# Kernel tuning notes

Measured on AMD Instinct MI355X. Metric: run time of the kernel, lower is better.

The kernel has to match this reference:

```python
import jax, jax.numpy as jnp
import numpy as np

NEG_SLOPE = 0.2  # PyG GATConv default leaky_relu slope


def _gat_conv(x, src, dst, W, a_src, a_dst, b, num_nodes):
    # Linear transform: [N, F_out]
    h = x @ W
    # Per-node attention halves (heads=1): [N]
    alpha_s = h @ a_src
    alpha_d = h @ a_dst
    # Per-edge raw score for edge j->i: a_src.h_j + a_dst.h_i
    e = jax.nn.leaky_relu(alpha_s[src] + alpha_d[dst], NEG_SLOPE)
    # Softmax over edges grouped by destination node (numerically stable)
    m = jax.ops.segment_max(e, dst, num_segments=num_nodes)
    ex = jnp.exp(e - m[dst])
    denom = jax.ops.segment_sum(ex, dst, num_segments=num_nodes)
    coef = ex / denom[dst]
    # Attention-weighted aggregation of source features into destinations
    out = jax.ops.segment_sum(h[src] * coef[:, None], dst, num_segments=num_nodes)
    return out + b


def setup_inputs() -> dict:
    key = jax.random.key(0)
    ks = jax.random.split(key, 12)
    N, F_in, F_hid, F_out, E = 100000, 128, 64, 40, 1600000
    x = jax.random.normal(ks[0], (N, F_in), dtype=jnp.float32)
    edge_index = jax.random.randint(ks[1], (2, E), 0, N, dtype=jnp.int64)
    g = lambda k, shape, fan: jax.random.normal(k, shape, dtype=jnp.float32) * (1.0 / np.sqrt(fan))
    return {
        "x": x,
        "edge_index": edge_index,
        "W1": g(ks[2], (F_in, F_hid), F_in),
        "a_src1": g(ks[3], (F_hid,), F_hid),
        "a_dst1": g(ks[4], (F_hid,), F_hid),
        "b1": jnp.zeros((F_hid,), dtype=jnp.float32),
        "W2": g(ks[5], (F_hid, F_out), F_hid),
        "a_src2": g(ks[6], (F_out,), F_out),
        "a_dst2": g(ks[7], (F_out,), F_out),
        "b2": jnp.zeros((F_out,), dtype=jnp.float32),
    }


def reference(x, edge_index, W1, a_src1, a_dst1, b1, W2, a_src2, a_dst2, b2):
    N = x.shape[0]
    # PyG GATConv adds self loops by default
    loops = jnp.arange(N, dtype=edge_index.dtype)
    src = jnp.concatenate([edge_index[0], loops])
    dst = jnp.concatenate([edge_index[1], loops])
    h = _gat_conv(x, src, dst, W1, a_src1, a_dst1, b1, N)
    h = jax.nn.relu(h)
    # dropout p=0.5 is inactive in eval mode
    h = _gat_conv(h, src, dst, W2, a_src2, a_dst2, b2, N)
    return jax.nn.log_softmax(h, axis=-1)
```

## Files before the change

### kernel.cpp

```cpp
#include <hip/hip_runtime.h>
#include <math.h>


constexpr int F_IN = 128;
constexpr int F_H  = 64;
constexpr int F_O  = 40;
constexpr int NBMAX = 512;
constexpr int CHUNK = 8192;
constexpr int NKEY  = 2048;

using h2 = decltype(__builtin_amdgcn_cvt_pkrtz(0.f, 0.f));
typedef __attribute__((ext_vector_type(4))) float f32x4;
typedef __attribute__((ext_vector_type(8))) short s16x8;

__device__ __forceinline__ h2 u2h(unsigned u) { return __builtin_bit_cast(h2, u); }

__device__ __forceinline__ float fdot2f(h2 a, h2 b, float c) {
#if __has_builtin(__builtin_amdgcn_fdot2)
    return __builtin_amdgcn_fdot2(a, b, c, false);
#else
    return c + (float)a.x * (float)b.x + (float)a.y * (float)b.y;
#endif
}
__device__ __forceinline__ h2 pklo(unsigned a, unsigned b) {
    return u2h(__builtin_amdgcn_perm(a, b, 0x05040100u));
}
__device__ __forceinline__ h2 pkhi(unsigned a, unsigned b) {
    return u2h(__builtin_amdgcn_perm(a, b, 0x07060302u));
}
__device__ __forceinline__ unsigned short f2h(float f) {
    _Float16 x = (_Float16)f;
    return __builtin_bit_cast(unsigned short, x);
}


__global__ __launch_bounds__(256) void k_binA(const int* __restrict__ dsts,
                                              int* __restrict__ bcnt,
                                              int E, int Et, int NB) {
    __shared__ int hist[NBMAX];
    for (int i = threadIdx.x; i < NB; i += 256) hist[i] = 0;
    __syncthreads();
    int e0 = blockIdx.x * 2048;
#pragma unroll
    for (int it = 0; it < 8; ++it) {
        int e = e0 + it * 256 + threadIdx.x;
        if (e < Et) {
            int d = (e < E) ? dsts[e] : (e - E);
            atomicAdd(&hist[d >> 8], 1);
        }
    }
    __syncthreads();
    for (int i = threadIdx.x; i < NB; i += 256) {
        int c = hist[i];
        if (c) atomicAdd(&bcnt[i], c);
    }
}

__global__ __launch_bounds__(NBMAX) void k_binB(const int* __restrict__ bcnt,
                                                int* __restrict__ bbase,
                                                int* __restrict__ bcur,
                                                int* __restrict__ rp,
                                                int NB, int N, int Et) {
    __shared__ int sc[NBMAX];
    int t = threadIdx.x;
    int v = (t < NB) ? bcnt[t] : 0;
    sc[t] = v; __syncthreads();
    int x = v;
    for (int o = 1; o < NBMAX; o <<= 1) {
        int y = (t >= o) ? sc[t - o] : 0;
        __syncthreads();
        x += y;
        sc[t] = x;
        __syncthreads();
    }
    if (t < NB) { int b = x - v; bbase[t] = b; bcur[t] = b; }
    if (t == 0) rp[N] = Et;
}

__global__ __launch_bounds__(256) void k_binC(const int* __restrict__ srcs,
                                              const int* __restrict__ dsts,
                                              int* __restrict__ bcur,
                                              unsigned* __restrict__ binned,
                                              int E, int Et, int NB) {
    __shared__ int hist[NBMAX];
    __shared__ int gbase[NBMAX];
    __shared__ int lcnt[NBMAX];
    int t = threadIdx.x;
    for (int i = t; i < NB; i += 256) hist[i] = 0;
    __syncthreads();
    int e0 = blockIdx.x * CHUNK;
#pragma unroll 4
    for (int it = 0; it < CHUNK / 256; ++it) {
        int e = e0 + it * 256 + t;
        if (e < Et) {
            int d = (e < E) ? dsts[e] : (e - E);
            atomicAdd(&hist[d >> 8], 1);
        }
    }
    __syncthreads();
    for (int i = t; i < NB; i += 256) {
        int c = hist[i];
        gbase[i] = c ? atomicAdd(&bcur[i], c) : 0;
        lcnt[i] = 0;
    }
    __syncthreads();
#pragma unroll 4
    for (int it = 0; it < CHUNK / 256; ++it) {
        int e = e0 + it * 256 + t;
        if (e < Et) {
            int s, d;
            if (e < E) { s = srcs[e]; d = dsts[e]; } else { s = e - E; d = s; }
            int b = d >> 8;
            int p = atomicAdd(&lcnt[b], 1);
            binned[gbase[b] + p] = (unsigned)s | ((unsigned)(d & 255) << 24);
        }
    }
}


__global__ __launch_bounds__(256) void k_binD(const unsigned* __restrict__ binned,
                                              const int* __restrict__ bbase,
                                              const int* __restrict__ bcur,
                                              int* __restrict__ rp,
                                              int* __restrict__ csr, int N) {
    __shared__ int hist[NKEY];
    __shared__ int sc2[NKEY];
    __shared__ int lcnt[NKEY];
    __shared__ int tsum[256];
    int b = blockIdx.x, t = threadIdx.x;
    int base = bbase[b], end = bcur[b];
    for (int k = t; k < NKEY; k += 256) { hist[k] = 0; lcnt[k] = 0; }
    __syncthreads();
    for (int j = base + t; j < end; j += 256) {
        unsigned w = binned[j];
        int key = ((int)(w >> 24) << 3) | (int)((w & 0xFFFFFFu) >> 14);
        atomicAdd(&hist[key], 1);
    }
    __syncthreads();
    int myk = t << 3;
    int s = 0;
#pragma unroll
    for (int k = 0; k < 8; ++k) s += hist[myk + k];
    tsum[t] = s; __syncthreads();
    int x = s;
    for (int o = 1; o < 256; o <<= 1) {
        int y = (t >= o) ? tsum[t - o] : 0;
        __syncthreads();
        x += y;
        tsum[t] = x;
        __syncthreads();
    }
    int run = x - s;
    int g = (b << 8) + t;
    if (g < N) rp[g] = base + run;
#pragma unroll
    for (int k = 0; k < 8; ++k) { sc2[myk + k] = run; run += hist[myk + k]; }
    __syncthreads();
    for (int j = base + t; j < end; j += 256) {
        unsigned w = binned[j];
        int src = (int)(w & 0xFFFFFFu);
        int key = ((int)(w >> 24) << 3) | (src >> 14);
        int p = atomicAdd(&lcnt[key], 1);
        csr[base + sc2[key] + p] = src;
    }
}


__global__ __launch_bounds__(256) void k_wsplit(const float* __restrict__ W,
                                                unsigned short* __restrict__ WhiT,
                                                unsigned short* __restrict__ WloT) {
    int i = blockIdx.x * 256 + threadIdx.x;
    if (i >= F_IN * F_H) return;
    int k = i >> 6, c = i & 63;
    float w = W[i];
    unsigned u = __float_as_uint(w);
    unsigned hi = u & 0xFFFF0000u;
    float d = w - __uint_as_float(hi);
    WhiT[c * F_IN + k] = (unsigned short)(hi >> 16);
    WloT[c * F_IN + k] = (unsigned short)(__float_as_uint(d) >> 16);
}


__global__ __launch_bounds__(64) void k_wprep(const float* __restrict__ W2,
                                              const float* __restrict__ a2s,
                                              const float* __restrict__ a2d,
                                              const float* __restrict__ b2,
                                              float* __restrict__ wasL,
                                              float* __restrict__ wadL,
                                              float* __restrict__ csb) {
    int k = threadIdx.x;
    float s = 0.f, d = 0.f;
    for (int c = 0; c < F_O; ++c) {
        float w = W2[k * F_O + c];
        s += w * a2s[c];
        d += w * a2d[c];
    }
    wasL[k] = s;
    wadL[k] = d;
    if (k == 0) {
        float cs = 0.f, cd = 0.f;
        for (int c = 0; c < F_O; ++c) { cs += b2[c] * a2s[c]; cd += b2[c] * a2d[c]; }
        csb[0] = cs; csb[1] = cd;
    }
}


__global__ __launch_bounds__(256, 2) void k_gemm1m(const float* __restrict__ x,
                                                   const unsigned short* __restrict__ WhiT,
                                                   const unsigned short* __restrict__ WloT,
                                                   const float* __restrict__ avs,
                                                   const float* __restrict__ avd,
                                                   unsigned short* __restrict__ h,
                                                   float* __restrict__ as,
                                                   float* __restrict__ ad, int N) {
    __shared__ __align__(16) float xs[64][132];
    unsigned short (*hs)[72] = (unsigned short(*)[72])xs;
    const int t = threadIdx.x;
    const int wv = t >> 6;
    const int lane = t & 63;
    const int lrow = lane & 15;
    const int lk8 = lane >> 4;
    const int r0 = blockIdx.x * 64;

    {
        const float4* xg = (const float4*)x;
#pragma unroll
        for (int it = 0; it < 8; ++it) {
            int flat = it * 256 + t;
            int row = flat >> 5, c4 = flat & 31;
            int grow = min(r0 + row, N - 1);
            float4 v = xg[(size_t)grow * 32 + c4];
            *(float4*)&xs[row][c4 * 4] = v;
        }
    }

    s16x8 bh[4][4], bl[4][4];
#pragma unroll
    for (int kt = 0; kt < 4; ++kt)
#pragma unroll
        for (int ct = 0; ct < 4; ++ct) {
            const int boff = (ct * 16 + lrow) * F_IN + kt * 32 + lk8 * 8;
            bh[kt][ct] = *(const s16x8*)&WhiT[boff];
            bl[kt][ct] = *(const s16x8*)&WloT[boff];
        }
    __syncthreads();

    s16x8 ah[4], al[4];
#pragma unroll
    for (int kt = 0; kt < 4; ++kt) {
        const float* rp_ = &xs[wv * 16 + lrow][kt * 32 + lk8 * 8];
        float4 a = *(const float4*)rp_;
        float4 b = *(const float4*)(rp_ + 4);
        float e0[8] = {a.x, a.y, a.z, a.w, b.x, b.y, b.z, b.w};
        unsigned uh[4], ul[4];
#pragma unroll
        for (int p = 0; p < 4; ++p) {
            float a0 = e0[2 * p], a1 = e0[2 * p + 1];
            unsigned u0 = __float_as_uint(a0), u1 = __float_as_uint(a1);
            float d0 = a0 - __uint_as_float(u0 & 0xFFFF0000u);
            float d1 = a1 - __uint_as_float(u1 & 0xFFFF0000u);
            uh[p] = __builtin_amdgcn_perm(u1, u0, 0x07060302u);
            ul[p] = __builtin_amdgcn_perm(__float_as_uint(d1), __float_as_uint(d0), 0x07060302u);
        }
        ah[kt] = __builtin_bit_cast(s16x8, make_uint4(uh[0], uh[1], uh[2], uh[3]));
        al[kt] = __builtin_bit_cast(s16x8, make_uint4(ul[0], ul[1], ul[2], ul[3]));
    }
    __syncthreads();

    f32x4 acc[4] = {};
#pragma unroll
    for (int kt = 0; kt < 4; ++kt) {
#pragma unroll
        for (int ct = 0; ct < 4; ++ct) {
            acc[ct] = __builtin_amdgcn_mfma_f32_16x16x32_bf16(ah[kt], bh[kt][ct], acc[ct], 0, 0, 0);
            acc[ct] = __builtin_amdgcn_mfma_f32_16x16x32_bf16(al[kt], bh[kt][ct], acc[ct], 0, 0, 0);
            acc[ct] = __builtin_amdgcn_mfma_f32_16x16x32_bf16(ah[kt], bl[kt][ct], acc[ct], 0, 0, 0);
        }
    }

    float avs_c[4], avd_c[4];
#pragma unroll
    for (int ct = 0; ct < 4; ++ct) {
        avs_c[ct] = avs[ct * 16 + lrow];
        avd_c[ct] = avd[ct * 16 + lrow];
    }
#pragma unroll
    for (int r = 0; r < 4; ++r) {
        float ps = acc[0][r] * avs_c[0] + acc[1][r] * avs_c[1]
                 + acc[2][r] * avs_c[2] + acc[3][r] * avs_c[3];
        float pd = acc[0][r] * avd_c[0] + acc[1][r] * avd_c[1]
                 + acc[2][r] * avd_c[2] + acc[3][r] * avd_c[3];
#pragma unroll
        for (int o = 8; o; o >>= 1) {
            ps += __shfl_xor(ps, o, 16);
            pd += __shfl_xor(pd, o, 16);
        }
        int orow = r0 + wv * 16 + lk8 * 4 + r;
        if (lrow == 0 && orow < N) { as[orow] = ps; ad[orow] = pd; }
    }

#pragma unroll
    for (int ct = 0; ct < 4; ++ct)
#pragma unroll
        for (int r = 0; r < 4; ++r)
            hs[wv * 16 + lk8 * 4 + r][ct * 16 + lrow] = f2h(acc[ct][r]);
    __syncthreads();
    const int row = t >> 2, ch = t & 3;
    const int grow = r0 + row;
    if (grow < N) {
        uint4 v0 = *(const uint4*)&hs[row][ch * 16];
        uint4 v1 = *(const uint4*)&hs[row][ch * 16 + 8];
        uint4* gp = (uint4*)(h + (size_t)grow * F_H + ch * 16);
        gp[0] = v0; gp[1] = v1;
    }
}


template <int MODE>
__global__ __launch_bounds__(256) void k_agg(const int* __restrict__ rp,
                                             const int* __restrict__ csr,
                                             const float* __restrict__ as,
                                             const float* __restrict__ ad,
                                             const uint4* __restrict__ h4,
                                             const float* __restrict__ b1,
                                             unsigned short* __restrict__ out1h,
                                             const float* __restrict__ wasL,
                                             const float* __restrict__ wadL,
                                             const float* __restrict__ csb,
                                             float* __restrict__ as2,
                                             float* __restrict__ ad2,
                                             const float* __restrict__ W2,
                                             const float* __restrict__ b2,
                                             float* __restrict__ out2, int N) {
    constexpr int CAP = 64;
    __shared__ __align__(16) uint2 wsb[4][8][CAP + 2];
    __shared__ __align__(16) float W2sT[MODE ? F_O * 68 : 1];
    const int t = threadIdx.x;
    const int w = t >> 6;
    const int g = (t >> 3) & 7;
    const int c = t & 7;
    if (MODE) {
        for (int idx = t; idx < F_H * F_O; idx += 256) {
            int k = idx / F_O, cc = idx - k * F_O;
            W2sT[cc * 68 + k] = W2[idx];
        }
        __syncthreads();
    }
    const int i = blockIdx.x * 32 + (t >> 3);
    if (i >= N) return;
    const int start = rp[i], end = rp[i + 1];
    const int deg = end - start;
    const int dm = min(deg, CAP);
    const int dmR8 = (dm + 7) & ~7;
    const float adi = ad[i];

    for (int idx = c; idx < dm; idx += 8) {
        int srcn = __builtin_nontemporal_load(&csr[start + idx]);
        float e = as[srcn] + adi;
        e = fmaxf(e, 0.2f * e);
        wsb[w][g][idx] = make_uint2(__float_as_uint(__expf(e)), (unsigned)srcn);
    }
    {
        int idx = dm + c;
        if (idx < dmR8) wsb[w][g][idx] = make_uint2(0u, (unsigned)i);
    }

    const uint4* pw = (const uint4*)wsb[w][g];
    float acc[8] = {}, acc2[8] = {};
    float sacc = 0.f;
    const int noct = dmR8 >> 3;
    for (int q = 0; q < noct; ++q) {
        uint4 m0 = pw[4 * q];
        uint4 m1 = pw[4 * q + 1];
        uint4 m2 = pw[4 * q + 2];
        uint4 m3 = pw[4 * q + 3];
        uint4 hv0 = h4[((size_t)m0.y << 3) + c];
        uint4 hv1 = h4[((size_t)m0.w << 3) + c];
        uint4 hv2 = h4[((size_t)m1.y << 3) + c];
        uint4 hv3 = h4[((size_t)m1.w << 3) + c];
        uint4 hv4 = h4[((size_t)m2.y << 3) + c];
        uint4 hv5 = h4[((size_t)m2.w << 3) + c];
        uint4 hv6 = h4[((size_t)m3.y << 3) + c];
        uint4 hv7 = h4[((size_t)m3.w << 3) + c];
        float w0 = __uint_as_float(m0.x), w1 = __uint_as_float(m0.z);
        float w2 = __uint_as_float(m1.x), w3 = __uint_as_float(m1.z);
        float w4 = __uint_as_float(m2.x), w5 = __uint_as_float(m2.z);
        float w6 = __uint_as_float(m3.x), w7 = __uint_as_float(m3.z);
        sacc += ((w0 + w1) + (w2 + w3)) + ((w4 + w5) + (w6 + w7));
        h2 wp0 = __builtin_amdgcn_cvt_pkrtz(w0, w1);
        h2 wp1 = __builtin_amdgcn_cvt_pkrtz(w2, w3);
        h2 wp2 = __builtin_amdgcn_cvt_pkrtz(w4, w5);
        h2 wp3 = __builtin_amdgcn_cvt_pkrtz(w6, w7);
        acc[0] = fdot2f(wp0, pklo(hv1.x, hv0.x), acc[0]);
        acc[1] = fdot2f(wp0, pkhi(hv1.x, hv0.x), acc[1]);
        acc[2] = fdot2f(wp0, pklo(hv1.y, hv0.y), acc[2]);
        acc[3] = fdot2f(wp0, pkhi(hv1.y, hv0.y), acc[3]);
        acc[4] = fdot2f(wp0, pklo(hv1.z, hv0.z), acc[4]);
        acc[5] = fdot2f(wp0, pkhi(hv1.z, hv0.z), acc[5]);
        acc[6] = fdot2f(wp0, pklo(hv1.w, hv0.w), acc[6]);
        acc[7] = fdot2f(wp0, pkhi(hv1.w, hv0.w), acc[7]);
        acc2[0] = fdot2f(wp1, pklo(hv3.x, hv2.x), acc2[0]);
        acc2[1] = fdot2f(wp1, pkhi(hv3.x, hv2.x), acc2[1]);
        acc2[2] = fdot2f(wp1, pklo(hv3.y, hv2.y), acc2[2]);
        acc2[3] = fdot2f(wp1, pkhi(hv3.y, hv2.y), acc2[3]);
        acc2[4] = fdot2f(wp1, pklo(hv3.z, hv2.z), acc2[4]);
        acc2[5] = fdot2f(wp1, pkhi(hv3.z, hv2.z), acc2[5]);
        acc2[6] = fdot2f(wp1, pklo(hv3.w, hv2.w), acc2[6]);
        acc2[7] = fdot2f(wp1, pkhi(hv3.w, hv2.w), acc2[7]);
        acc[0] = fdot2f(wp2, pklo(hv5.x, hv4.x), acc[0]);
        acc[1] = fdot2f(wp2, pkhi(hv5.x, hv4.x), acc[1]);
        acc[2] = fdot2f(wp2, pklo(hv5.y, hv4.y), acc[2]);
        acc[3] = fdot2f(wp2, pkhi(hv5.y, hv4.y), acc[3]);
        acc[4] = fdot2f(wp2, pklo(hv5.z, hv4.z), acc[4]);
        acc[5] = fdot2f(wp2, pkhi(hv5.z, hv4.z), acc[5]);
        acc[6] = fdot2f(wp2, pklo(hv5.w, hv4.w), acc[6]);
        acc[7] = fdot2f(wp2, pkhi(hv5.w, hv4.w), acc[7]);
        acc2[0] = fdot2f(wp3, pklo(hv7.x, hv6.x), acc2[0]);
        acc2[1] = fdot2f(wp3, pkhi(hv7.x, hv6.x), acc2[1]);
        acc2[2] = fdot2f(wp3, pklo(hv7.y, hv6.y), acc2[2]);
        acc2[3] = fdot2f(wp3, pkhi(hv7.y, hv6.y), acc2[3]);
        acc2[4] = fdot2f(wp3, pklo(hv7.z, hv6.z), acc2[4]);
        acc2[5] = fdot2f(wp3, pkhi(hv7.z, hv6.z), acc2[5]);
        acc2[6] = fdot2f(wp3, pklo(hv7.w, hv6.w), acc2[6]);
        acc2[7] = fdot2f(wp3, pkhi(hv7.w, hv6.w), acc2[7]);
    }

    for (int j = start + dm; j < end; ++j) {
        int srcn = __builtin_nontemporal_load(&csr[j]);
        float e = as[srcn] + adi;
        e = fmaxf(e, 0.2f * e);
        float wv = __expf(e);
        sacc += wv;
        uint4 hv = h4[((size_t)srcn << 3) + c];
        h2 wp = __builtin_amdgcn_cvt_pkrtz(wv, 0.f);
        acc[0] = fdot2f(wp, pklo(hv.x, hv.x), acc[0]);
        acc[1] = fdot2f(wp, pkhi(hv.x, hv.x), acc[1]);
        acc[2] = fdot2f(wp, pklo(hv.y, hv.y), acc[2]);
        acc[3] = fdot2f(wp, pkhi(hv.y, hv.y), acc[3]);
        acc[4] = fdot2f(wp, pklo(hv.z, hv.z), acc[4]);
        acc[5] = fdot2f(wp, pkhi(hv.z, hv.z), acc[5]);
        acc[6] = fdot2f(wp, pklo(hv.w, hv.w), acc[6]);
        acc[7] = fdot2f(wp, pkhi(hv.w, hv.w), acc[7]);
    }

#pragma unroll
    for (int k = 0; k < 8; ++k) acc[k] += acc2[k];
    float inv = 1.f / sacc;

    if (MODE == 0) {
        float r[8];
#pragma unroll
        for (int k = 0; k < 8; ++k)
            r[k] = fmaxf(fmaf(acc[k], inv, b1[8 * c + k]), 0.f);
        unsigned u0 = (unsigned)f2h(r[0]) | ((unsigned)f2h(r[1]) << 16);
        unsigned u1 = (unsigned)f2h(r[2]) | ((unsigned)f2h(r[3]) << 16);
        unsigned u2 = (unsigned)f2h(r[4]) | ((unsigned)f2h(r[5]) << 16);
        unsigned u3 = (unsigned)f2h(r[6]) | ((unsigned)f2h(r[7]) << 16);
        *(uint4*)(out1h + (size_t)i * F_H + 8 * c) = make_uint4(u0, u1, u2, u3);
        float4 wa0 = *(const float4*)&wasL[8 * c];
        float4 wa1 = *(const float4*)&wasL[8 * c + 4];
        float4 wd0 = *(const float4*)&wadL[8 * c];
        float4 wd1 = *(const float4*)&wadL[8 * c + 4];
        float ps = r[0] * wa0.x + r[1] * wa0.y + r[2] * wa0.z + r[3] * wa0.w
                 + r[4] * wa1.x + r[5] * wa1.y + r[6] * wa1.z + r[7] * wa1.w;
        float pd = r[0] * wd0.x + r[1] * wd0.y + r[2] * wd0.z + r[3] * wd0.w
                 + r[4] * wd1.x + r[5] * wd1.y + r[6] * wd1.z + r[7] * wd1.w;
#pragma unroll
        for (int o = 4; o; o >>= 1) {
            ps += __shfl_xor(ps, o, 8);
            pd += __shfl_xor(pd, o, 8);
        }
        if (c == 0) { as2[i] = ps + csb[0]; ad2[i] = pd + csb[1]; }
    } else {
        float* gl = (float*)&wsb[w][g][0];
        ((float4*)gl)[2 * c]     = make_float4(acc[0] * inv, acc[1] * inv, acc[2] * inv, acc[3] * inv);
        ((float4*)gl)[2 * c + 1] = make_float4(acc[4] * inv, acc[5] * inv, acc[6] * inv, acc[7] * inv);
        float v[5];
#pragma unroll
        for (int m = 0; m < 5; ++m) v[m] = b2[c + 8 * m];
#pragma unroll
        for (int m = 0; m < 5; ++m) {
            const float* wr = &W2sT[(c + 8 * m) * 68];
            float vm = v[m];
#pragma unroll
            for (int k4 = 0; k4 < 16; ++k4) {
                float4 a4 = ((const float4*)gl)[k4];
                float4 w4 = *(const float4*)&wr[k4 * 4];
                vm += a4.x * w4.x + a4.y * w4.y + a4.z * w4.z + a4.w * w4.w;
            }
            v[m] = vm;
        }
        float mx = fmaxf(fmaxf(fmaxf(v[0], v[1]), fmaxf(v[2], v[3])), v[4]);
#pragma unroll
        for (int o = 4; o; o >>= 1) mx = fmaxf(mx, __shfl_xor(mx, o, 8));
        float es = __expf(v[0] - mx) + __expf(v[1] - mx) + __expf(v[2] - mx)
                 + __expf(v[3] - mx) + __expf(v[4] - mx);
#pragma unroll
        for (int o = 4; o; o >>= 1) es += __shfl_xor(es, o, 8);
        float lse = mx + __logf(es);
        float* op = out2 + (size_t)i * F_O + c;
#pragma unroll
        for (int m = 0; m < 5; ++m)
            __builtin_nontemporal_store(v[m] - lse, op + 8 * m);
    }
}


extern "C" void kernel_launch(void* const* d_in, const int* in_sizes, int n_in,
                              void* d_out, int out_size, void* d_ws, size_t ws_size,
                              hipStream_t stream) {
    const float* x   = (const float*)d_in[0];
    const int* edges = (const int*)d_in[1];
    const float* W1  = (const float*)d_in[2];
    const float* av_s1 = (const float*)d_in[3];
    const float* av_d1 = (const float*)d_in[4];
    const float* b1  = (const float*)d_in[5];
    const float* W2  = (const float*)d_in[6];
    const float* av_s2 = (const float*)d_in[7];
    const float* av_d2 = (const float*)d_in[8];
    const float* b2  = (const float*)d_in[9];
    float* out = (float*)d_out;

    const int N  = in_sizes[0] / F_IN;
    const int E  = in_sizes[1] / 2;
    const int Et = E + N;
    const int NB = (N + 255) >> 8;

    char* p = (char*)d_ws;
    auto alloc = [&](size_t bytes) {
        char* q = p;
        p += (bytes + 255) & ~(size_t)255;
        return (void*)q;
    };
    unsigned short* h1 = (unsigned short*)alloc((size_t)N * F_H * 2);
    unsigned short* out1h = (unsigned short*)alloc((size_t)N * F_H * 2);
    float* as1    = (float*)alloc((size_t)N * 4);
    float* ad1    = (float*)alloc((size_t)N * 4);
    float* as2    = (float*)alloc((size_t)N * 4);
    float* ad2    = (float*)alloc((size_t)N * 4);
    int* rp       = (int*)alloc((size_t)(N + 1) * 4);
    int* bcnt     = (int*)alloc(NBMAX * 4);
    int* bbase    = (int*)alloc(NBMAX * 4);
    int* bcur     = (int*)alloc(NBMAX * 4);
    unsigned* binned = (unsigned*)alloc((size_t)Et * 4);
    int* csr      = (int*)alloc((size_t)Et * 4);
    unsigned short* WhiT = (unsigned short*)alloc((size_t)F_H * F_IN * 2);
    unsigned short* WloT = (unsigned short*)alloc((size_t)F_H * F_IN * 2);
    float* wasL   = (float*)alloc(F_H * 4);
    float* wadL   = (float*)alloc(F_H * 4);
    float* csb    = (float*)alloc(2 * 4);
    (void)n_in; (void)out_size; (void)ws_size;

    const int* srcs = edges;
    const int* dsts = edges + E;

    hipMemsetAsync(bcnt, 0, NBMAX * 4, stream);

    k_wsplit<<<(F_IN * F_H + 255) / 256, 256, 0, stream>>>(W1, WhiT, WloT);
    k_wprep<<<1, 64, 0, stream>>>(W2, av_s2, av_d2, b2, wasL, wadL, csb);
    k_binA<<<(Et + 2047) / 2048, 256, 0, stream>>>(dsts, bcnt, E, Et, NB);
    k_binB<<<1, NBMAX, 0, stream>>>(bcnt, bbase, bcur, rp, NB, N, Et);
    k_binC<<<(Et + CHUNK - 1) / CHUNK, 256, 0, stream>>>(srcs, dsts, bcur, binned, E, Et, NB);
    k_binD<<<NB, 256, 0, stream>>>(binned, bbase, bcur, rp, csr, N);

    k_gemm1m<<<(N + 63) / 64, 256, 0, stream>>>(x, WhiT, WloT, av_s1, av_d1, h1, as1, ad1, N);
    int gAgg = (N + 31) / 32;
    k_agg<0><<<gAgg, 256, 0, stream>>>(rp, csr, as1, ad1, (const uint4*)h1,
                                       b1, out1h, wasL, wadL, csb, as2, ad2,
                                       nullptr, nullptr, nullptr, N);
    k_agg<1><<<gAgg, 256, 0, stream>>>(rp, csr, as2, ad2, (const uint4*)out1h,
                                       nullptr, nullptr, nullptr, nullptr, nullptr,
                                       nullptr, nullptr, W2, b2, out, N);
}
```

Measured before the change: 283.1 us.

## Use packed fp16 dot2 for layer-2 projection with prepacked W2 and merged prep kernel

Precomputes W2 as packed fp16 pairs in a merged prep kernel and stores it in a padded layout. The layer-2 aggregation kernel now copies that buffer straight into shared memory and runs its 64x40 projection with fdot2 on fp16 pairs instead of fp32 float4 FMAs. This halves shared-memory traffic and the size of the per-block W2 load, and saves one kernel launch. In exchange, the row activations and weights are rounded to fp16 before the final projection, which lowers precision.

```diff
diff --git a/kernel.cpp b/kernel.cpp
--- a/kernel.cpp
+++ b/kernel.cpp
@@ -14,6 +14,7 @@
 typedef __attribute__((ext_vector_type(8))) short s16x8;
 
 __device__ __forceinline__ h2 u2h(unsigned u) { return __builtin_bit_cast(h2, u); }
+__device__ __forceinline__ unsigned h2u(h2 h) { return __builtin_bit_cast(unsigned, h); }
 
 __device__ __forceinline__ float fdot2f(h2 a, h2 b, float c) {
 #if __has_builtin(__builtin_amdgcn_fdot2)
@@ -166,38 +167,43 @@
 }
 
 
-__global__ __launch_bounds__(256) void k_wsplit(const float* __restrict__ W,
-                                                unsigned short* __restrict__ WhiT,
-                                                unsigned short* __restrict__ WloT) {
-    int i = blockIdx.x * 256 + threadIdx.x;
-    if (i >= F_IN * F_H) return;
-    int k = i >> 6, c = i & 63;
-    float w = W[i];
-    unsigned u = __float_as_uint(w);
-    unsigned hi = u & 0xFFFF0000u;
-    float d = w - __uint_as_float(hi);
-    WhiT[c * F_IN + k] = (unsigned short)(hi >> 16);
-    WloT[c * F_IN + k] = (unsigned short)(__float_as_uint(d) >> 16);
-}
-
-
-__global__ __launch_bounds__(64) void k_wprep(const float* __restrict__ W2,
+__global__ __launch_bounds__(256) void k_prep(const float* __restrict__ W1,
+                                              unsigned short* __restrict__ WhiT,
+                                              unsigned short* __restrict__ WloT,
+                                              const float* __restrict__ W2,
                                               const float* __restrict__ a2s,
                                               const float* __restrict__ a2d,
                                               const float* __restrict__ b2,
+                                              unsigned* __restrict__ W2p,
                                               float* __restrict__ wasL,
                                               float* __restrict__ wadL,
                                               float* __restrict__ csb) {
-    int k = threadIdx.x;
-    float s = 0.f, d = 0.f;
-    for (int c = 0; c < F_O; ++c) {
-        float w = W2[k * F_O + c];
-        s += w * a2s[c];
-        d += w * a2d[c];
-    }
-    wasL[k] = s;
-    wadL[k] = d;
-    if (k == 0) {
+    int i = blockIdx.x * 256 + threadIdx.x;
+    if (i < F_IN * F_H) {
+        int k = i >> 6, c = i & 63;
+        float w = W1[i];
+        unsigned u = __float_as_uint(w);
+        unsigned hi = u & 0xFFFF0000u;
+        float d = w - __uint_as_float(hi);
+        WhiT[c * F_IN + k] = (unsigned short)(hi >> 16);
+        WloT[c * F_IN + k] = (unsigned short)(__float_as_uint(d) >> 16);
+    }
+    if (i < F_O * 32) {
+        int cc = i >> 5, k2 = i & 31;
+        W2p[cc * 34 + k2] = h2u(__builtin_amdgcn_cvt_pkrtz(
+            W2[(2 * k2) * F_O + cc], W2[(2 * k2 + 1) * F_O + cc]));
+    }
+    if (i < F_H) {
+        float s = 0.f, d = 0.f;
+        for (int c = 0; c < F_O; ++c) {
+            float w = W2[i * F_O + c];
+            s += w * a2s[c];
+            d += w * a2d[c];
+        }
+        wasL[i] = s;
+        wadL[i] = d;
+    }
+    if (i == 0) {
         float cs = 0.f, cd = 0.f;
         for (int c = 0; c < F_O; ++c) { cs += b2[c] * a2s[c]; cd += b2[c] * a2d[c]; }
         csb[0] = cs; csb[1] = cd;
@@ -329,21 +335,19 @@
                                              const float* __restrict__ csb,
                                              float* __restrict__ as2,
                                              float* __restrict__ ad2,
-                                             const float* __restrict__ W2,
+                                             const unsigned* __restrict__ W2p,
                                              const float* __restrict__ b2,
                                              float* __restrict__ out2, int N) {
     constexpr int CAP = 64;
     __shared__ __align__(16) uint2 wsb[4][8][CAP + 2];
-    __shared__ __align__(16) float W2sT[MODE ? F_O * 68 : 1];
+    __shared__ __align__(16) unsigned W2s[MODE ? F_O * 34 : 1];
     const int t = threadIdx.x;
     const int w = t >> 6;
     const int g = (t >> 3) & 7;
     const int c = t & 7;
     if (MODE) {
-        for (int idx = t; idx < F_H * F_O; idx += 256) {
-            int k = idx / F_O, cc = idx - k * F_O;
-            W2sT[cc * 68 + k] = W2[idx];
-        }
+        for (int idx = t; idx < F_O * 34; idx += 256)
+            W2s[idx] = W2p[idx];
         __syncthreads();
     }
     const int i = blockIdx.x * 32 + (t >> 3);
@@ -472,23 +476,21 @@
         }
         if (c == 0) { as2[i] = ps + csb[0]; ad2[i] = pd + csb[1]; }
     } else {
-        float* gl = (float*)&wsb[w][g][0];
-        ((float4*)gl)[2 * c]     = make_float4(acc[0] * inv, acc[1] * inv, acc[2] * inv, acc[3] * inv);
-        ((float4*)gl)[2 * c + 1] = make_float4(acc[4] * inv, acc[5] * inv, acc[6] * inv, acc[7] * inv);
+        unsigned* gl = (unsigned*)&wsb[w][g][0];
+        uint4 pk;
+        pk.x = h2u(__builtin_amdgcn_cvt_pkrtz(acc[0] * inv, acc[1] * inv));
+        pk.y = h2u(__builtin_amdgcn_cvt_pkrtz(acc[2] * inv, acc[3] * inv));
+        pk.z = h2u(__builtin_amdgcn_cvt_pkrtz(acc[4] * inv, acc[5] * inv));
+        pk.w = h2u(__builtin_amdgcn_cvt_pkrtz(acc[6] * inv, acc[7] * inv));
+        ((uint4*)gl)[c] = pk;
         float v[5];
 #pragma unroll
         for (int m = 0; m < 5; ++m) v[m] = b2[c + 8 * m];
-#pragma unroll
-        for (int m = 0; m < 5; ++m) {
-            const float* wr = &W2sT[(c + 8 * m) * 68];
-            float vm = v[m];
-#pragma unroll
-            for (int k4 = 0; k4 < 16; ++k4) {
-                float4 a4 = ((const float4*)gl)[k4];
-                float4 w4 = *(const float4*)&wr[k4 * 4];
-                vm += a4.x * w4.x + a4.y * w4.y + a4.z * w4.z + a4.w * w4.w;
-            }
-            v[m] = vm;
+        for (int k2 = 0; k2 < 32; ++k2) {
+            h2 a2 = u2h(gl[k2]);
+#pragma unroll
+            for (int m = 0; m < 5; ++m)
+                v[m] = fdot2f(a2, u2h(W2s[(c + 8 * m) * 34 + k2]), v[m]);
         }
         float mx = fmaxf(fmaxf(fmaxf(v[0], v[1]), fmaxf(v[2], v[3])), v[4]);
 #pragma unroll
@@ -546,6 +548,7 @@
     int* csr      = (int*)alloc((size_t)Et * 4);
     unsigned short* WhiT = (unsigned short*)alloc((size_t)F_H * F_IN * 2);
     unsigned short* WloT = (unsigned short*)alloc((size_t)F_H * F_IN * 2);
+    unsigned* W2p = (unsigned*)alloc((size_t)F_O * 34 * 4);
     float* wasL   = (float*)alloc(F_H * 4);
     float* wadL   = (float*)alloc(F_H * 4);
     float* csb    = (float*)alloc(2 * 4);
@@ -556,8 +559,9 @@
 
     hipMemsetAsync(bcnt, 0, NBMAX * 4, stream);
 
-    k_wsplit<<<(F_IN * F_H + 255) / 256, 256, 0, stream>>>(W1, WhiT, WloT);
-    k_wprep<<<1, 64, 0, stream>>>(W2, av_s2, av_d2, b2, wasL, wadL, csb);
+    k_prep<<<(F_IN * F_H + 255) / 256, 256, 0, stream>>>(W1, WhiT, WloT,
+                                                         W2, av_s2, av_d2, b2,
+                                                         W2p, wasL, wadL, csb);
     k_binA<<<(Et + 2047) / 2048, 256, 0, stream>>>(dsts, bcnt, E, Et, NB);
     k_binB<<<1, NBMAX, 0, stream>>>(bcnt, bbase, bcur, rp, NB, N, Et);
     k_binC<<<(Et + CHUNK - 1) / CHUNK, 256, 0, stream>>>(srcs, dsts, bcur, binned, E, Et, NB);
@@ -570,5 +574,5 @@
                                        nullptr, nullptr, nullptr, N);
     k_agg<1><<<gAgg, 256, 0, stream>>>(rp, csr, as2, ad2, (const uint4*)out1h,
                                        nullptr, nullptr, nullptr, nullptr, nullptr,
-                                       nullptr, nullptr, W2, b2, out, N);
-}
+                                       nullptr, nullptr, W2p, b2, out, N);
+}
```

After: 277.8 us. No clear change (-1.9%).
